# Optimization experiments

Measured on AMD Instinct MI355X. Metric: run time of the kernel, lower is better.

The kernel has to match this reference:

```python
import jax, jax.numpy as jnp
import numpy as np

L = 12      # n_layers
C = 768     # n_embd = dim = dim_att
H = 12      # heads
N = 64      # head_size_a
FF = 2688   # dim_ffn = int(768*3.5//32*32)
P = 2       # patch_size
INCH = 4
IMG = 32
NCLS = 1000
FREQ = 256
HC = C // 2  # conv stem channels (dim//2)
B = 32
D_MIX = 32
D_DEC = 64
LNX_EPS = 1e-5 * 8.0 ** 2  # GroupNorm eps with head_size_divisor=8


def _ln(x, w=None, b=None, eps=1e-5):
    m = x.mean(-1, keepdims=True)
    v = x.var(-1, keepdims=True)
    xh = (x - m) * jax.lax.rsqrt(v + eps)
    if w is not None:
        xh = xh * w + b
    return xh


def _shift(x):  # RWKV token shift: prepend zero row, drop last
    return jnp.pad(x, ((0, 0), (1, 0), (0, 0)))[:, :-1]


def _gn_img(x, w, b, groups=32, eps=1e-5):
    Bb, Ch, Hh, Ww = x.shape
    xg = x.reshape(Bb, groups, Ch // groups, Hh, Ww)
    m = xg.mean((2, 3, 4), keepdims=True)
    v = xg.var((2, 3, 4), keepdims=True)
    xg = (xg - m) * jax.lax.rsqrt(v + eps)
    return xg.reshape(Bb, Ch, Hh, Ww) * w[None, :, None, None] + b[None, :, None, None]


def _conv5(x, w, b):
    y = jax.lax.conv_general_dilated(x, w, (1, 1), ((2, 2), (2, 2)),
                                     dimension_numbers=('NCHW', 'OIHW', 'NCHW'))
    return y + b[None, :, None, None]


def _wkv(r, k, v, w, u):
    # r,k,v,w: (B,T,H,N); u: (H,N). S[b,h,i,j]: key i -> value j.
    def step(S, inp):
        rt, kt, vt, wt = inp  # each (B,H,N)
        kv = kt[..., :, None] * vt[..., None, :]           # (B,H,N,N)
        y = jnp.einsum('bhi,bhij->bhj', rt, S + u[None, :, :, None] * kv)
        S = wt[..., :, None] * S + kv
        return S, y
    S0 = jnp.zeros((r.shape[0], H, N, N), r.dtype)
    seq = tuple(jnp.moveaxis(a, 1, 0) for a in (r, k, v, w))
    _, ys = jax.lax.scan(step, S0, seq)
    return jnp.moveaxis(ys, 0, 1)  # (B,T,H,N)


def _timemix(x, p):
    Bb, Tt, _ = x.shape
    xx = _shift(x) - x
    xxx = x + xx * p['maa'][0]
    mix = jnp.tanh(xxx @ p['tm_w1']).reshape(Bb, Tt, 5, D_MIX)
    m = jnp.einsum('btfd,fdc->fbtc', mix, p['tm_w2'])  # (5,B,T,C): mw,mk,mv,mr,mg
    xw = x + xx * (p['maa'][1] + m[0])
    xk = x + xx * (p['maa'][2] + m[1])
    xv = x + xx * (p['maa'][3] + m[2])
    xr = x + xx * (p['maa'][4] + m[3])
    xg = x + xx * (p['maa'][5] + m[4])
    r = (xr @ p['r_w'].T).reshape(Bb, Tt, H, N)
    k = (xk @ p['k_w'].T).reshape(Bb, Tt, H, N)
    v = (xv @ p['v_w'].T).reshape(Bb, Tt, H, N)
    g = jax.nn.silu(xg @ p['g_w'].T)
    ww = p['td'] + jnp.tanh(xw @ p['td_w1']) @ p['td_w2']
    w = jnp.exp(-jnp.exp(ww)).reshape(Bb, Tt, H, N)
    y = _wkv(r, k, v, w, p['faaaa'])  # (B,T,H,N)
    mn = y.mean(-1, keepdims=True)
    vr = y.var(-1, keepdims=True)
    y = ((y - mn) * jax.lax.rsqrt(vr + LNX_EPS)).reshape(Bb, Tt, C) * p['lnx_w'] + p['lnx_b']
    return (y * g) @ p['o_w'].T


def _chanmix(x, p):
    xx = _shift(x) - x
    xk = x + xx * p['fmaa'][0]
    xr = x + xx * p['fmaa'][1]
    k = jnp.square(jax.nn.relu(xk @ p['fk_w'].T))
    return jax.nn.sigmoid(xr @ p['fr_w'].T) * (k @ p['fv_w'].T)


def _forward(x, t, y, c1_w, c1_b, gn1_w, gn1_b, c2_w, c2_b, gn2_w, gn2_b,
             xe_w, xe_b, te_w1, te_b1, te_w2, te_b2, y_tab, ln0_w, ln0_b,
             ln1_w, ln1_b, ln2_w, ln2_b, att_maa, tm_w1, tm_w2, td, td_w1,
             td_w2, faaaa, r_w, k_w, v_w, o_w, g_w, lnx_w, lnx_b, ffn_maa,
             fk_w, fr_w, fv_w, ada_w, ada_b, fl_ada_w, fl_ada_b, fl_w, fl_b):
    Bb = x.shape[0]
    h = jax.nn.silu(_conv5(x, c1_w, c1_b))
    h = _gn_img(h, gn1_w, gn1_b)
    h = jax.nn.silu(_conv5(h, c2_w, c2_b))
    h = _gn_img(h, gn2_w, gn2_b)
    # patchify: (B,HC,IMG,IMG) -> (B,T,P*P*HC)
    G = IMG // P
    h = h.reshape(Bb, HC, G, P, G, P).transpose(0, 2, 4, 1, 3, 5).reshape(Bb, G * G, HC * P * P)
    xs = h @ xe_w.T + xe_b
    # timestep embedding
    half = FREQ // 2
    freqs = jnp.exp(-jnp.log(10000.0) * jnp.arange(half, dtype=jnp.float32) / half)
    ang = t[:, None] * freqs[None]
    temb = jnp.concatenate([jnp.cos(ang), jnp.sin(ang)], -1)
    temb = jax.nn.silu(temb @ te_w1.T + te_b1) @ te_w2.T + te_b2
    c = temb + y_tab[y]  # adaln_input (B,C)
    for l in range(L):
        ada = jax.nn.silu(c) @ ada_w[l].T + ada_b[l]
        sm, scm, gm, sp, scp, gp = jnp.split(ada, 6, axis=1)
        if l == 0:
            xs = _ln(xs, ln0_w, ln0_b)
        p = dict(maa=att_maa[l], tm_w1=tm_w1[l], tm_w2=tm_w2[l], td=td[l],
                 td_w1=td_w1[l], td_w2=td_w2[l], faaaa=faaaa[l], r_w=r_w[l],
                 k_w=k_w[l], v_w=v_w[l], o_w=o_w[l], g_w=g_w[l], lnx_w=lnx_w[l],
                 lnx_b=lnx_b[l], fmaa=ffn_maa[l], fk_w=fk_w[l], fr_w=fr_w[l],
                 fv_w=fv_w[l])
        hmod = _ln(xs, ln1_w[l], ln1_b[l]) * (1 + scm[:, None, :]) + sm[:, None, :]
        xs = xs + gm[:, None, :] * _timemix(hmod, p)
        hmod = _ln(xs, ln2_w[l], ln2_b[l]) * (1 + scp[:, None, :]) + sp[:, None, :]
        xs = xs + gp[:, None, :] * _chanmix(hmod, p)
    ada = jax.nn.silu(c) @ fl_ada_w.T + fl_ada_b
    sh, sc = jnp.split(ada, 2, axis=1)
    out = (_ln(xs, eps=1e-6) * (1 + sc[:, None, :]) + sh[:, None, :]) @ fl_w.T + fl_b
    G = IMG // P
    out = out.reshape(Bb, G, G, P, P, INCH)
    out = jnp.einsum('nhwpqc->nchpwq', out).reshape(Bb, INCH, IMG, IMG)
    return out


def setup_inputs() -> dict:
    key = jax.random.key(0)
    ks = iter(jax.random.split(key, 64))
    def rn(shape, s=0.02):
        return (jax.random.normal(next(ks), shape) * s).astype(jnp.float32)
    inp = {}
    inp['x'] = jax.random.normal(next(ks), (B, INCH, IMG, IMG), jnp.float32)
    inp['t'] = jax.random.uniform(next(ks), (B,), jnp.float32) * 1000.0
    inp['y'] = jax.random.randint(next(ks), (B,), 0, NCLS)
    inp['c1_w'] = rn((HC, INCH, 5, 5), 0.05); inp['c1_b'] = jnp.zeros(HC)
    inp['gn1_w'] = jnp.ones(HC); inp['gn1_b'] = jnp.zeros(HC)
    inp['c2_w'] = rn((HC, HC, 5, 5), 0.02); inp['c2_b'] = jnp.zeros(HC)
    inp['gn2_w'] = jnp.ones(HC); inp['gn2_b'] = jnp.zeros(HC)
    inp['xe_w'] = rn((C, P * P * HC)); inp['xe_b'] = jnp.zeros(C)
    inp['te_w1'] = rn((C, FREQ)); inp['te_b1'] = jnp.zeros(C)
    inp['te_w2'] = rn((C, C)); inp['te_b2'] = jnp.zeros(C)
    inp['y_tab'] = rn((NCLS + 1, C))
    inp['ln0_w'] = jnp.ones(C); inp['ln0_b'] = jnp.zeros(C)
    inp['ln1_w'] = jnp.ones((L, C)); inp['ln1_b'] = jnp.zeros((L, C))
    inp['ln2_w'] = jnp.ones((L, C)); inp['ln2_b'] = jnp.zeros((L, C))
    inp['att_maa'] = jax.random.uniform(next(ks), (L, 6, C), jnp.float32)
    inp['tm_w1'] = rn((L, C, 5 * D_MIX), 0.01)
    inp['tm_w2'] = rn((L, 5, D_MIX, C), 0.01)
    inp['td'] = rn((L, C), 0.5) - 3.0
    inp['td_w1'] = rn((L, C, D_DEC), 0.01)
    inp['td_w2'] = rn((L, D_DEC, C), 0.01)
    inp['faaaa'] = rn((L, H, N), 0.1)
    for nm in ('r_w', 'k_w', 'v_w', 'o_w', 'g_w'):
        inp[nm] = rn((L, C, C))
    inp['lnx_w'] = jnp.ones((L, C)); inp['lnx_b'] = jnp.zeros((L, C))
    inp['ffn_maa'] = jax.random.uniform(next(ks), (L, 2, C), jnp.float32)
    inp['fk_w'] = rn((L, FF, C)); inp['fr_w'] = rn((L, C, C)); inp['fv_w'] = rn((L, C, FF))
    inp['ada_w'] = rn((L, 6 * C, C)); inp['ada_b'] = jnp.zeros((L, 6 * C))
    inp['fl_ada_w'] = rn((2 * C, C)); inp['fl_ada_b'] = jnp.zeros(2 * C)
    inp['fl_w'] = rn((P * P * INCH, C)); inp['fl_b'] = jnp.zeros(P * P * INCH)
    return inp


def reference(x, t, y, c1_w, c1_b, gn1_w, gn1_b, c2_w, c2_b, gn2_w, gn2_b,
              xe_w, xe_b, te_w1, te_b1, te_w2, te_b2, y_tab, ln0_w, ln0_b,
              ln1_w, ln1_b, ln2_w, ln2_b, att_maa, tm_w1, tm_w2, td, td_w1,
              td_w2, faaaa, r_w, k_w, v_w, o_w, g_w, lnx_w, lnx_b, ffn_maa,
              fk_w, fr_w, fv_w, ada_w, ada_b, fl_ada_w, fl_ada_b, fl_w, fl_b):
    return _forward(x, t, y, c1_w, c1_b, gn1_w, gn1_b, c2_w, c2_b, gn2_w, gn2_b,
                    xe_w, xe_b, te_w1, te_b1, te_w2, te_b2, y_tab, ln0_w, ln0_b,
                    ln1_w, ln1_b, ln2_w, ln2_b, att_maa, tm_w1, tm_w2, td, td_w1,
                    td_w2, faaaa, r_w, k_w, v_w, o_w, g_w, lnx_w, lnx_b, ffn_maa,
                    fk_w, fr_w, fv_w, ada_w, ada_b, fl_ada_w, fl_ada_b, fl_w, fl_b)
```

## Files before the change

### kernel.cpp

```cpp
#include <hip/hip_runtime.h>
#include <math.h>


typedef short  s16x8 __attribute__((ext_vector_type(8)));
typedef float  f32x4 __attribute__((ext_vector_type(4)));
typedef __attribute__((address_space(1))) const void as1_cv;
typedef __attribute__((address_space(3))) void as3_v;

#define GLDS16(gp, lp) __builtin_amdgcn_global_load_lds( \
    (as1_cv*)(unsigned long long)(const void*)(gp), \
    (as3_v*)(unsigned int)(unsigned long long)(void*)(lp), 16, 0, 0)

static __device__ __forceinline__ float sigf(float x){ return 1.f/(1.f+expf(-x)); }
static __device__ __forceinline__ unsigned short f2b(float x){
  unsigned int u = __builtin_bit_cast(unsigned int, x);
  unsigned int r = (u + 0x7FFFu + ((u >> 16) & 1u)) >> 16;
  return (unsigned short)r;
}
static __device__ __forceinline__ float b2f(unsigned short h){
  unsigned int u = ((unsigned int)h)<<16; return __builtin_bit_cast(float,u);
}

static const size_t O_XS    = 0ull;
static const size_t O_HMOD  = 6291456ull;
static const size_t O_ADA   = 12582912ull;
static const size_t O_FLA   = 14352384ull;
static const size_t O_T2    = 14401536ull;
static const size_t O_SC    = 14426112ull;
static const size_t O_TI    = 14450688ull;
static const size_t O_T1    = 14458880ull;
static const size_t O_ST1   = 14483456ull;
static const size_t O_ST2   = 14485504ull;
static const size_t O_XEW16 = 14487552ull;
static const size_t O_WL16  = 15077376ull;
static const size_t O_BIG   = 19083264ull;
static const size_t L_XW    = 0ull;
static const size_t L_XX    = 6291456ull;
static const size_t L_XXX   = 12582912ull;
static const size_t L_KB    = 18874368ull;
static const size_t L_VB    = 25165824ull;
static const size_t L_GB    = 31457280ull;
static const size_t L_WD    = 37748736ull;
static const size_t L_MIXB  = 50331648ull;
static const size_t L_WT    = 51642368ull;
static const size_t L_XK16  = 52166656ull;
static const size_t L_XV16  = 55312384ull;
static const size_t L_XR16  = 58458112ull;
static const size_t L_XG16  = 61603840ull;
static const size_t L_GNH16 = 64749568ull;
static const size_t L_KBIG16= 67895296ull;
static const size_t S_IMG1  = 0ull;
static const size_t S_IMG2  = 12582912ull;
static const size_t S_PAD16 = 25165824ull;
static const size_t S_WTAP16= 33128448ull;
static const size_t S_PM16  = 34971648ull;

enum { EPI_NONE=0, EPI_SILU=1 };

template<int EPI, bool TB>
__global__ __launch_bounds__(256) void gemm_k(
    const float* __restrict__ A, const float* __restrict__ B,
    float* __restrict__ C, const float* __restrict__ bias,
    int M, int N, int K)
{
  __shared__ __align__(16) float As[16][68];
  __shared__ __align__(16) float Bs[16][68];
  const int tid = threadIdx.x;
  const int tx = tid & 15, ty = tid >> 4;
  const int row0 = blockIdx.y * 64, col0 = blockIdx.x * 64;
  const int lr = tid >> 2;
  const int lk = (tid & 3) << 2;
  float acc[4][4] = {};
  for (int k0 = 0; k0 < K; k0 += 16) {
    {
      int gr = row0 + lr;
      float4 v = make_float4(0.f,0.f,0.f,0.f);
      if (gr < M) v = *reinterpret_cast<const float4*>(A + (size_t)gr*K + (k0 + lk));
      As[lk+0][lr]=v.x; As[lk+1][lr]=v.y; As[lk+2][lr]=v.z; As[lk+3][lr]=v.w;
    }
    if (TB) {
      int gr = col0 + lr;
      float4 v = make_float4(0.f,0.f,0.f,0.f);
      if (gr < N) v = *reinterpret_cast<const float4*>(B + (size_t)gr*K + (k0 + lk));
      Bs[lk+0][lr]=v.x; Bs[lk+1][lr]=v.y; Bs[lk+2][lr]=v.z; Bs[lk+3][lr]=v.w;
    } else {
      int kr = tid >> 4;
      int gc = col0 + ((tid & 15) << 2);
      float4 v = make_float4(0.f,0.f,0.f,0.f);
      if (gc < N) v = *reinterpret_cast<const float4*>(B + (size_t)(k0+kr)*N + gc);
      Bs[kr][((tid&15)<<2)+0]=v.x; Bs[kr][((tid&15)<<2)+1]=v.y;
      Bs[kr][((tid&15)<<2)+2]=v.z; Bs[kr][((tid&15)<<2)+3]=v.w;
    }
    __syncthreads();
    #pragma unroll
    for (int kk=0;kk<16;kk++){
      const float4 a4 = *reinterpret_cast<const float4*>(&As[kk][ty<<2]);
      const float4 b4 = *reinterpret_cast<const float4*>(&Bs[kk][tx<<2]);
      const float av[4]={a4.x,a4.y,a4.z,a4.w};
      const float bv[4]={b4.x,b4.y,b4.z,b4.w};
      #pragma unroll
      for (int i=0;i<4;i++)
        #pragma unroll
        for (int j=0;j<4;j++)
          acc[i][j]=fmaf(av[i],bv[j],acc[i][j]);
    }
    __syncthreads();
  }
  #pragma unroll
  for (int i=0;i<4;i++){
    const int r = row0 + (ty<<2) + i;
    if (r >= M) break;
    #pragma unroll
    for (int j=0;j<4;j++){
      const int c = col0 + (tx<<2) + j;
      if (c >= N) break;
      float v = acc[i][j];
      if (bias) v += bias[c];
      const size_t idx = (size_t)r*N + c;
      if (EPI==EPI_NONE)        C[idx]=v;
      else if (EPI==EPI_SILU)   C[idx]=v*sigf(v);
    }
  }
}

#define GEMM(EPI,TB,A,B,C,bias,M,N,K) \
  gemm_k<EPI,TB><<<dim3(((N)+63)/64,((M)+63)/64),dim3(256),0,stream>>>((A),(B),(C),(bias),(M),(N),(K))

enum { BEPI_F32=0, BEPI_BIAS_F32, BEPI_SILU_F32, BEPI_SIG_F32, BEPI_RELU2_BF16,
       BEPI_RES_GM, BEPI_RES_GP, BEPI_TANH_BF16, BEPI_WDEC_F32 };

template<int EPI>
__global__ __launch_bounds__(256) void bgemm_k(
    const unsigned short* __restrict__ A, const unsigned short* __restrict__ B,
    void* __restrict__ Cv, const float* __restrict__ bias,
    const float* __restrict__ p1, const float* __restrict__ p2, int pstride,
    int M, int N, int K)
{
  __shared__ __align__(16) unsigned short As[128][64];
  __shared__ __align__(16) unsigned short Bs[128][64];
  const int tid = threadIdx.x;
  const int w = tid >> 6, lane = tid & 63;
  const int row0 = blockIdx.y * 128, col0 = blockIdx.x * 128;
  const int wr = w >> 1, wc = w & 1;
  const int l15 = lane & 15, l4 = lane >> 4;
  const int kkc = ((lane & 7) ^ (lane >> 3)) * 8;
  f32x4 acc[4][4] = {};
  for (int k0 = 0; k0 < K; k0 += 64) {
    #pragma unroll
    for (int i = 0; i < 4; i++) {
      const int rb = i*32 + w*8;
      const int r  = rb + (lane >> 3);
      GLDS16(A + (size_t)(row0 + r)*K + k0 + kkc, &As[rb][0]);
      GLDS16(B + (size_t)(col0 + r)*K + k0 + kkc, &Bs[rb][0]);
    }
    __syncthreads();
    #pragma unroll
    for (int ks = 0; ks < 2; ks++) {
      s16x8 af[4], bf[4];
      #pragma unroll
      for (int m = 0; m < 4; m++) {
        const int r = wr*64 + m*16 + l15;
        const int sl = (ks*4 + l4) ^ (r & 7);
        af[m] = *reinterpret_cast<const s16x8*>(&As[r][sl*8]);
      }
      #pragma unroll
      for (int n = 0; n < 4; n++) {
        const int r = wc*64 + n*16 + l15;
        const int sl = (ks*4 + l4) ^ (r & 7);
        bf[n] = *reinterpret_cast<const s16x8*>(&Bs[r][sl*8]);
      }
      #pragma unroll
      for (int m = 0; m < 4; m++)
        #pragma unroll
        for (int n = 0; n < 4; n++)
          acc[m][n] = __builtin_amdgcn_mfma_f32_16x16x32_bf16(af[m], bf[n], acc[m][n], 0, 0, 0);
    }
    __syncthreads();
  }
  float* Cf = (float*)Cv; unsigned short* Ch = (unsigned short*)Cv;
  #pragma unroll
  for (int m = 0; m < 4; m++) {
    const int rbase = row0 + wr*64 + m*16 + (l4<<2);
    #pragma unroll
    for (int n = 0; n < 4; n++) {
      const int c = col0 + wc*64 + n*16 + l15;
      if (c >= N) continue;
      #pragma unroll
      for (int q = 0; q < 4; q++) {
        const int r = rbase + q;
        const int bb = r >> 8;
        float v = acc[m][n][q];
        const size_t idx = (size_t)r*N + c;
        if (EPI==BEPI_F32)            Cf[idx] = v;
        else if (EPI==BEPI_BIAS_F32)  Cf[idx] = v + bias[c];
        else if (EPI==BEPI_SILU_F32)  Cf[idx] = v*sigf(v);
        else if (EPI==BEPI_SIG_F32)   Cf[idx] = sigf(v);
        else if (EPI==BEPI_RELU2_BF16){ float t=fmaxf(v,0.f); Ch[idx] = f2b(t*t); }
        else if (EPI==BEPI_RES_GM)    Cf[idx] += p1[(size_t)bb*pstride + c]*v;
        else if (EPI==BEPI_RES_GP)    Cf[idx] += p1[(size_t)bb*pstride + c]*(p2[idx]*v);
        else if (EPI==BEPI_TANH_BF16) Ch[idx] = f2b(tanhf(v));
        else if (EPI==BEPI_WDEC_F32)  Cf[idx] = expf(-expf(v + p1[c]));
      }
    }
  }
}

#define BGEMM(EPI,A16,B16,Cp,bias,p1,p2,ps,M,N,K) \
  bgemm_k<EPI><<<dim3(((N)+127)/128,(M)/128),dim3(256),0,stream>>>( \
    (const unsigned short*)(A16),(const unsigned short*)(B16),(void*)(Cp),(bias),(p1),(p2),(ps),(M),(N),(K))

struct BGrp { const unsigned short* A; const unsigned short* B; void* C;
              int epi; int N; int gx; };
struct BGrp4 { BGrp g[4]; };

__global__ __launch_bounds__(256) void bgemm_grp_k(BGrp4 G, int M, int K)
{
  const BGrp gr = G.g[blockIdx.z];
  if ((int)blockIdx.x >= gr.gx) return;
  __shared__ __align__(16) unsigned short As[128][64];
  __shared__ __align__(16) unsigned short Bs[128][64];
  const int tid = threadIdx.x;
  const int w = tid >> 6, lane = tid & 63;
  const int row0 = blockIdx.y * 128, col0 = blockIdx.x * 128;
  const int wr = w >> 1, wc = w & 1;
  const int l15 = lane & 15, l4 = lane >> 4;
  const int kkc = ((lane & 7) ^ (lane >> 3)) * 8;
  const int N = gr.N;
  f32x4 acc[4][4] = {};
  for (int k0 = 0; k0 < K; k0 += 64) {
    #pragma unroll
    for (int i = 0; i < 4; i++) {
      const int rb = i*32 + w*8;
      const int r  = rb + (lane >> 3);
      GLDS16(gr.A + (size_t)(row0 + r)*K + k0 + kkc, &As[rb][0]);
      GLDS16(gr.B + (size_t)(col0 + r)*K + k0 + kkc, &Bs[rb][0]);
    }
    __syncthreads();
    #pragma unroll
    for (int ks = 0; ks < 2; ks++) {
      s16x8 af[4], bf[4];
      #pragma unroll
      for (int m = 0; m < 4; m++) {
        const int r = wr*64 + m*16 + l15;
        const int sl = (ks*4 + l4) ^ (r & 7);
        af[m] = *reinterpret_cast<const s16x8*>(&As[r][sl*8]);
      }
      #pragma unroll
      for (int n = 0; n < 4; n++) {
        const int r = wc*64 + n*16 + l15;
        const int sl = (ks*4 + l4) ^ (r & 7);
        bf[n] = *reinterpret_cast<const s16x8*>(&Bs[r][sl*8]);
      }
      #pragma unroll
      for (int m = 0; m < 4; m++)
        #pragma unroll
        for (int n = 0; n < 4; n++)
          acc[m][n] = __builtin_amdgcn_mfma_f32_16x16x32_bf16(af[m], bf[n], acc[m][n], 0, 0, 0);
    }
    __syncthreads();
  }
  float* Cf = (float*)gr.C; unsigned short* Ch = (unsigned short*)gr.C;
  #pragma unroll
  for (int m = 0; m < 4; m++) {
    const int rbase = row0 + wr*64 + m*16 + (l4<<2);
    #pragma unroll
    for (int n = 0; n < 4; n++) {
      const int c = col0 + wc*64 + n*16 + l15;
      #pragma unroll
      for (int q = 0; q < 4; q++) {
        const int r = rbase + q;
        float v = acc[m][n][q];
        const size_t idx = (size_t)r*N + c;
        switch (gr.epi) {
          case 0: Cf[idx] = v; break;
          case 1: Cf[idx] = v*sigf(v); break;
          case 2: Cf[idx] = sigf(v); break;
          case 3: { float t=fmaxf(v,0.f); Ch[idx] = f2b(t*t); } break;
          case 4: Ch[idx] = f2b(v); break;
          default: Ch[idx] = f2b(v*sigf(v)); break;
        }
      }
    }
  }
}

__global__ __launch_bounds__(256) void conv1_k(
    const float* __restrict__ x, const float* __restrict__ w,
    const float* __restrict__ bias, float* __restrict__ out)
{
  const int blk = blockIdx.x; const int bb = blk / 384; const int oc = blk % 384;
  __shared__ __align__(16) float sIn[4*1296];
  __shared__ __align__(16) float sW[100];
  const int tid = threadIdx.x;
  for (int idx=tid; idx<4*1296; idx+=256){
    int ic = idx/1296; int rem = idx - ic*1296;
    int yy = rem/36, xx = rem - yy*36;
    int gy = yy-2, gx = xx-2;
    float v = 0.f;
    if ((unsigned)gy < 32u && (unsigned)gx < 32u)
      v = x[(((size_t)bb*4+ic)*32+gy)*32+gx];
    sIn[idx]=v;
  }
  if (tid < 100) sW[tid] = w[(size_t)oc*100 + tid];
  __syncthreads();
  const float bv = bias[oc];
  #pragma unroll
  for (int i=0;i<4;i++){
    int p = tid + 256*i; int py=p>>5, px=p&31;
    int pb = py*36+px;
    float acc = bv;
    #pragma unroll
    for (int ic=0;ic<4;ic++)
      #pragma unroll
      for (int ky=0;ky<5;ky++)
        #pragma unroll
        for (int kx=0;kx<5;kx++)
          acc = fmaf(sIn[ic*1296 + pb + ky*36+kx], sW[ic*25+ky*5+kx], acc);
    out[((size_t)(bb*384+oc))*1024 + p] = acc*sigf(acc);
  }
}

__global__ __launch_bounds__(256) void gn_stats_nchw_k(
    const float* __restrict__ h, float* __restrict__ stats)
{
  const int blk = blockIdx.x;
  const size_t base = (size_t)blk*12288;
  const int tid = threadIdx.x;
  float s=0.f, s2=0.f;
  for (int idx=tid; idx<12288; idx+=256){ float v=h[base+idx]; s+=v; s2=fmaf(v,v,s2); }
  #pragma unroll
  for (int mask=32; mask>=1; mask>>=1){ s += __shfl_xor(s,mask); s2 += __shfl_xor(s2,mask); }
  __shared__ float ps[8];
// ... 5 lines not shown
    float var  = s2*(1.f/12288.f) - mean*mean;
    stats[blk*2] = mean; stats[blk*2+1] = rsqrtf(var + 1e-5f);
  }
}

__global__ void zero16_k(unsigned short* __restrict__ p)
{
  size_t i = ((size_t)blockIdx.x*256 + threadIdx.x)*8;
  *reinterpret_cast<uint4*>(p + i) = make_uint4(0u,0u,0u,0u);
}

__global__ __launch_bounds__(256) void pad_apply_k(
    const float* __restrict__ img1, const float* __restrict__ stats,
    const float* __restrict__ w, const float* __restrict__ bgn,
    unsigned short* __restrict__ pad)
{
  __shared__ float t[8][33];
  const int b = blockIdx.x >> 5, y = blockIdx.x & 31;
  const int tid = threadIdx.x;
  for (int ic0 = 0; ic0 < 384; ic0 += 8) {
    const int icr = tid >> 5, xr = tid & 31;
    t[icr][xr] = img1[(((size_t)b*384 + ic0+icr)*32 + y)*32 + xr];
    __syncthreads();
    const int xw_ = tid >> 3, icw = tid & 7;
    const int ch = ic0 + icw;
    const int g = ch / 12;
    const float mean = stats[(b*32+g)*2], rstd = stats[(b*32+g)*2+1];
    float v = (t[icw][xw_] - mean)*rstd*w[ch] + bgn[ch];
    pad[(((size_t)b*36 + y+2)*36 + (xw_+2))*384 + ch] = f2b(v);
    __syncthreads();
  }
}

__global__ __launch_bounds__(256) void wrepack_k(
    const float* __restrict__ w, unsigned short* __restrict__ wtap)
{
  __shared__ float t[9600];
  const int oc = blockIdx.x; const int tid = threadIdx.x;
  for (int i=tid;i<9600;i+=256) t[i] = w[(size_t)oc*9600 + i];
  __syncthreads();
  for (int i=tid;i<9600;i+=256){
    int tap=i/384, ic=i-tap*384;
    wtap[((size_t)tap*384 + oc)*384 + ic] = f2b(t[ic*25+tap]);
  }
}

__global__ __launch_bounds__(256) void conv2m_k(
    const unsigned short* __restrict__ inp,
    const unsigned short* __restrict__ wtap,
    const float* __restrict__ bias, unsigned short* __restrict__ out)
{
  __shared__ __align__(16) unsigned short As[128][64];
  __shared__ __align__(16) unsigned short Bs[128][64];
  const int blk = blockIdx.x;
  const int b = blk / 24, rem = blk % 24, pt = rem / 3, ot = rem % 3;
  const int y0 = pt * 4, oc0 = ot * 128;
  const int tid = threadIdx.x, w = tid>>6, lane = tid&63;
  const int wr = w>>1, wc = w&1;
  const int l15 = lane & 15, l4 = lane >> 4;
  const int kkc = ((lane&7) ^ (lane>>3)) * 8;
  f32x4 acc[4][4] = {};
  for (int ic0 = 0; ic0 < 384; ic0 += 64) {
    for (int dy = 0; dy < 5; dy++) {
      for (int dx = 0; dx < 5; dx++) {
        const int tap = dy*5 + dx;
        #pragma unroll
        for (int i = 0; i < 4; i++) {
          const int rb = i*32 + w*8;
          const int r = rb + (lane>>3);
          const int py = r >> 5, px = r & 31;
          GLDS16(inp + (((size_t)(b*36 + y0+py+dy))*36 + (px+dx))*384 + ic0 + kkc, &As[rb][0]);
          GLDS16(wtap + ((size_t)tap*384 + oc0 + r)*384 + ic0 + kkc, &Bs[rb][0]);
        }
        __syncthreads();
        #pragma unroll
        for (int ks = 0; ks < 2; ks++) {
          s16x8 af[4], bf[4];
          #pragma unroll
          for (int m = 0; m < 4; m++) {
            const int r = wr*64 + m*16 + l15;
            const int sl = (ks*4 + l4) ^ (r & 7);
            af[m] = *reinterpret_cast<const s16x8*>(&As[r][sl*8]);
          }
          #pragma unroll
          for (int n = 0; n < 4; n++) {
            const int r = wc*64 + n*16 + l15;
            const int sl = (ks*4 + l4) ^ (r & 7);
            bf[n] = *reinterpret_cast<const s16x8*>(&Bs[r][sl*8]);
          }
          #pragma unroll
          for (int m = 0; m < 4; m++)
            #pragma unroll
            for (int n = 0; n < 4; n++)
              acc[m][n] = __builtin_amdgcn_mfma_f32_16x16x32_bf16(af[m], bf[n], acc[m][n], 0, 0, 0);
        }
        __syncthreads();
      }
    }
  }
  #pragma unroll
  for (int m = 0; m < 4; m++) {
    #pragma unroll
    for (int n = 0; n < 4; n++) {
      const int oc = oc0 + wc*64 + n*16 + l15;
      const float bv = bias[oc];
      #pragma unroll
      for (int q = 0; q < 4; q++) {
        const int p = wr*64 + m*16 + (l4<<2) + q;
// ... 148 lines not shown
__global__ __launch_bounds__(256) void ln_shift_cm_k(
    const float* __restrict__ xs, const float* __restrict__ w, const float* __restrict__ b,
    const float* __restrict__ mod, const float* __restrict__ fmaa,
    unsigned short* __restrict__ xk16, unsigned short* __restrict__ xr16)
{
  const int m = blockIdx.x, tid = threadIdx.x;
  const size_t base = (size_t)m*768;
  const int t = m & 255, bb = m >> 8;
  float c0=xs[base+tid], c1=xs[base+tid+256], c2=xs[base+tid+512];
  float p0=0.f,p1=0.f,p2=0.f;
  if (t) { p0=xs[base-768+tid]; p1=xs[base-512+tid]; p2=xs[base-256+tid]; }
  float sc_=c0+c1+c2, sc2=fmaf(c0,c0,fmaf(c1,c1,c2*c2));
  float sp_=p0+p1+p2, sp2=fmaf(p0,p0,fmaf(p1,p1,p2*p2));
  #pragma unroll
  for (int mask=32; mask>=1; mask>>=1){
    sc_+=__shfl_xor(sc_,mask); sc2+=__shfl_xor(sc2,mask);
    sp_+=__shfl_xor(sp_,mask); sp2+=__shfl_xor(sp2,mask);
  }
  __shared__ float ps[16];
  if ((tid&63)==0){ int wv=tid>>6; ps[wv]=sc_; ps[4+wv]=sc2; ps[8+wv]=sp_; ps[12+wv]=sp2; }
  __syncthreads();
  sc_=ps[0]+ps[1]+ps[2]+ps[3]; sc2=ps[4]+ps[5]+ps[6]+ps[7];
  sp_=ps[8]+ps[9]+ps[10]+ps[11]; sp2=ps[12]+ps[13]+ps[14]+ps[15];
  const float mc = sc_*(1.f/768.f), rc = rsqrtf(sc2*(1.f/768.f)-mc*mc + 1e-5f);
  const float mp = sp_*(1.f/768.f), rp = rsqrtf(sp2*(1.f/768.f)-mp*mp + 1e-5f);
  #pragma unroll
  for (int k=0;k<3;k++){
    const int c = tid + k*256;
    const float scv = mod[(size_t)bb*55296 + 3072 + c];
    const float shv = mod[(size_t)bb*55296 + 2304 + c];
    float cv = (k==0)?c0:((k==1)?c1:c2);
    float h = fmaf((cv-mc)*rc, w[c], b[c]);
    h = fmaf(h, 1.f+scv, shv);
    float pv = 0.f;
    if (t) {
      float pk = (k==0)?p0:((k==1)?p1:p2);
      pv = fmaf((pk-mp)*rp, w[c], b[c]);
      pv = fmaf(pv, 1.f+scv, shv);
    }
    const float d = pv - h;
    xk16[base+c] = f2b(fmaf(d, fmaa[c], h));
    xr16[base+c] = f2b(fmaf(d, fmaa[768+c], h));
  }
}

__global__ __launch_bounds__(256) void five_mix_k(
    const unsigned short* __restrict__ mix16, const float* __restrict__ w2,
    const float* __restrict__ hmod, const float* __restrict__ xx,
    const float* __restrict__ maa15,
    unsigned short* __restrict__ xw, unsigned short* __restrict__ xk,
    unsigned short* __restrict__ xv, unsigned short* __restrict__ xr,
    unsigned short* __restrict__ xg)
{
  __shared__ __align__(16) float smix[16][160];
  const int m0 = blockIdx.x * 16;
  const int tid = threadIdx.x;
  for (int idx=tid; idx<16*160; idx+=256){
    int r = idx/160, d = idx - r*160;
    smix[r][d] = b2f(mix16[(size_t)(m0+r)*160 + d]);
  }
  __syncthreads();
  #pragma unroll 1
  for (int cc=0; cc<3; cc++){
    const int c = tid + cc*256;
    float hv[16], xv_[16];
    #pragma unroll
    for (int r=0;r<16;r++){ size_t id=(size_t)(m0+r)*768+c; hv[r]=hmod[id]; xv_[r]=xx[id]; }
    #pragma unroll 1
    for (int f=0; f<5; f++){
      float acc[16];
      const float base = maa15[f*768 + c];
      #pragma unroll
      for (int r=0;r<16;r++) acc[r]=base;
      #pragma unroll 1
      for (int d4=0; d4<8; d4++){
        float wv[4];
        #pragma unroll
        for (int q=0;q<4;q++) wv[q] = w2[(size_t)(f*32+d4*4+q)*768 + c];
        #pragma unroll
        for (int r=0;r<16;r++){
          const float4 mv = *reinterpret_cast<const float4*>(&smix[r][f*32+d4*4]);
          acc[r] = fmaf(mv.x,wv[0],fmaf(mv.y,wv[1],fmaf(mv.z,wv[2],fmaf(mv.w,wv[3],acc[r]))));
        }
      }
      #pragma unroll
      for (int r=0;r<16;r++){
        float val = fmaf(xv_[r], acc[r], hv[r]);
        size_t id = (size_t)(m0+r)*768+c;
        if (f==0) xw[id]=f2b(val);
        else if (f==1) xk[id]=f2b(val);
        else if (f==2) xv[id]=f2b(val);
        else if (f==3) xr[id]=f2b(val);
        else           xg[id]=f2b(val);
      }
    }
  }
}

__global__ __launch_bounds__(256) void wkv_k(
    const unsigned short* __restrict__ rg, const unsigned short* __restrict__ kg,
    const unsigned short* __restrict__ vg, const float* __restrict__ wg,
    const unsigned short* __restrict__ gg, const float* __restrict__ u,
    const float* __restrict__ lnxw, const float* __restrict__ lnxb,
    unsigned short* __restrict__ out16)
{
  const int bh = blockIdx.x; const int b = bh/12, h = bh%12;
  const int tid = threadIdx.x;
  const int w = tid >> 6, lane = tid & 63;
  const int l4 = lane >> 4, l15 = lane & 15;
  __shared__ __align__(16) unsigned short r16s[32][64], k16s[32][64], v16s[32][64], g16s[32][64];
  __shared__ __align__(16) float wds[32][64];
  __shared__ __align__(16) float Wl[33][64];
  __shared__ __align__(16) unsigned short rr16[32][64], kk16[32][64];
  __shared__ __align__(16) unsigned short kk2T[64][32], vT[64][32];
  __shared__ __align__(16) unsigned short S16T[64][64];
  __shared__ __align__(16) unsigned short A16[32][32];
  __shared__ float diag[32], ypsum[32][4], ypsq[32][4];

  reinterpret_cast<uint4*>(&S16T[0][0])[tid] = make_uint4(0,0,0,0);
  reinterpret_cast<uint4*>(&S16T[0][0])[256+tid] = make_uint4(0,0,0,0);

  const float u_lane = u[h*64 + lane];
  const int jj = w*16 + l15;
  const float lw = lnxw[h*64 + jj], lb = lnxb[h*64 + jj];
  const size_t gb = (size_t)(b*256)*768 + h*64;

  const int st_t = tid >> 3, st_i = (tid & 7) * 8;
  uint4 pr, pk, pv, pg; float4 pw0, pw1;

#define WKV_LOADC(c_) { \
    const size_t tb = gb + (size_t)((c_)*32 + st_t)*768 + st_i; \
    pr = *reinterpret_cast<const uint4*>(rg + tb); \
    pk = *reinterpret_cast<const uint4*>(kg + tb); \
    pv = *reinterpret_cast<const uint4*>(vg + tb); \
    pg = *reinterpret_cast<const uint4*>(gg + tb); \
    pw0 = *reinterpret_cast<const float4*>(wg + tb); \
    pw1 = *reinterpret_cast<const float4*>(wg + tb + 4); }
#define WKV_STAGE() { \
    *reinterpret_cast<uint4*>(&r16s[st_t][st_i]) = pr; \
// ... 126 lines not shown
    }
    #pragma unroll
    for (int m=0;m<2;m++)
      #pragma unroll
      for (int q=0;q<4;q++){
        float s1 = Y[m][q], s2 = s1*s1;
        #pragma unroll
        for (int mask=8; mask>=1; mask>>=1){ s1 += __shfl_xor(s1,mask); s2 += __shfl_xor(s2,mask); }
        if (l15==0){ const int t = m*16 + l4*4 + q; ypsum[t][w]=s1; ypsq[t][w]=s2; }
      }
    __syncthreads();
    #pragma unroll
    for (int m=0;m<2;m++)
      #pragma unroll
      for (int q=0;q<4;q++){
        const int t = m*16 + l4*4 + q;
        float s1 = ypsum[t][0]+ypsum[t][1]+ypsum[t][2]+ypsum[t][3];
        float s2 = ypsq[t][0]+ypsq[t][1]+ypsq[t][2]+ypsq[t][3];
        float mean = s1*(1.f/64.f);
        float var  = s2*(1.f/64.f) - mean*mean;
        float xh = (Y[m][q]-mean)*rsqrtf(var + 6.4e-4f);
        float o = fmaf(xh, lw, lb) * b2f(g16s[t][jj]);
        out16[gb + (size_t)(c*32+t)*768 + jj] = f2b(o);
      }
    if (c < 7) {
      __syncthreads();
      WKV_STAGE();
      __syncthreads();
    }
  }
#undef WKV_LOADC
#undef WKV_STAGE
}

__global__ void unpatch_k(const float* __restrict__ po, float* __restrict__ out)
{
  int idx = blockIdx.x*256 + threadIdx.x;
  int xq=idx&31; int yy=(idx>>5)&31; int ch=(idx>>10)&3; int bb=idx>>12;
  int gh=yy>>1, p=yy&1, gw=xq>>1, q=xq&1;
  out[idx] = po[((size_t)(bb*256+gh*16+gw))*16 + p*8+q*4+ch];
}

__global__ void f2b_k(const float* __restrict__ s, unsigned short* __restrict__ d)
{
  size_t i = ((size_t)blockIdx.x*256 + threadIdx.x)*8;
  float4 a = *reinterpret_cast<const float4*>(s+i);
  float4 b = *reinterpret_cast<const float4*>(s+i+4);
  s16x8 o;
  o[0]=(short)f2b(a.x); o[1]=(short)f2b(a.y); o[2]=(short)f2b(a.z); o[3]=(short)f2b(a.w);
  o[4]=(short)f2b(b.x); o[5]=(short)f2b(b.y); o[6]=(short)f2b(b.z); o[7]=(short)f2b(b.w);
  *reinterpret_cast<s16x8*>(d + i) = o;
}

__global__ void f2b_layer_k(
    const float* __restrict__ r_, const float* __restrict__ k_, const float* __restrict__ v_,
    const float* __restrict__ o_, const float* __restrict__ g_, const float* __restrict__ fr_,
    const float* __restrict__ fk_, const float* __restrict__ fv_,
    unsigned short* __restrict__ dst)
{
  size_t i = ((size_t)blockIdx.x*256 + threadIdx.x)*8;
  const float* s; size_t off;
  if (i < 3538944) {
    unsigned seg = (unsigned)(i / 589824u); off = i - (size_t)seg*589824u;
    s = seg==0?r_:seg==1?k_:seg==2?v_:seg==3?o_:seg==4?g_:fr_;
  } else if (i < 5603328) { s = fk_; off = i - 3538944; }
  else                    { s = fv_; off = i - 5603328; }
  float4 a = *reinterpret_cast<const float4*>(s+off);
  float4 b = *reinterpret_cast<const float4*>(s+off+4);
  s16x8 o;
  o[0]=(short)f2b(a.x); o[1]=(short)f2b(a.y); o[2]=(short)f2b(a.z); o[3]=(short)f2b(a.w);
  o[4]=(short)f2b(b.x); o[5]=(short)f2b(b.y); o[6]=(short)f2b(b.z); o[7]=(short)f2b(b.w);
  *reinterpret_cast<s16x8*>(dst + i) = o;
}

__global__ void wmix_repack_k(const float* __restrict__ tm1, const float* __restrict__ td1,
                              const float* __restrict__ td2, unsigned short* __restrict__ dst)
{
  int idx = blockIdx.x*256 + threadIdx.x;
  if (idx < 196608) {
    int n = idx/768, k = idx - n*768;
    dst[idx] = (n<160) ? f2b(tm1[(size_t)k*160 + n]) : (unsigned short)0;
  } else if (idx < 294912) {
    int i = idx-196608; int n = i/768, k = i - n*768;
    dst[idx] = (n<64) ? f2b(td1[(size_t)k*64 + n]) : (unsigned short)0;
  } else {
    int i = idx-294912; int n = i/64, k = i - n*64;
    dst[idx] = f2b(td2[(size_t)k*768 + n]);
  }
}

extern "C" void kernel_launch(void* const* d_in, const int* in_sizes, int n_in,
                              void* d_out, int out_size, void* d_ws, size_t ws_size,
                              hipStream_t stream)
{
  const float* x_in  = (const float*)d_in[0];
  const float* t_in  = (const float*)d_in[1];
  const int*   y_in  = (const int*)  d_in[2];
  const float* c1w   = (const float*)d_in[3];
  const float* c1b   = (const float*)d_in[4];
  const float* gn1w  = (const float*)d_in[5];
  const float* gn1b  = (const float*)d_in[6];
  const float* c2w   = (const float*)d_in[7];
  const float* c2b   = (const float*)d_in[8];
  const float* gn2w  = (const float*)d_in[9];
  const float* gn2b  = (const float*)d_in[10];
  const float* xew   = (const float*)d_in[11];
  const float* xeb   = (const float*)d_in[12];
  const float* tew1  = (const float*)d_in[13];
  const float* teb1  = (const float*)d_in[14];
  const float* tew2  = (const float*)d_in[15];
  const float* teb2  = (const float*)d_in[16];
  const float* ytab  = (const float*)d_in[17];
  const float* ln0w  = (const float*)d_in[18];
  const float* ln0b  = (const float*)d_in[19];
  const float* ln1w  = (const float*)d_in[20];
  const float* ln1b  = (const float*)d_in[21];
  const float* ln2w  = (const float*)d_in[22];
  const float* ln2b  = (const float*)d_in[23];
  const float* amaa  = (const float*)d_in[24];
  const float* tmw1  = (const float*)d_in[25];
  const float* tmw2  = (const float*)d_in[26];
  const float* tdv   = (const float*)d_in[27];
  const float* tdw1  = (const float*)d_in[28];
  const float* tdw2  = (const float*)d_in[29];
  const float* faa   = (const float*)d_in[30];
  const float* rw    = (const float*)d_in[31];
  const float* kw    = (const float*)d_in[32];
  const float* vw    = (const float*)d_in[33];
  const float* ow    = (const float*)d_in[34];
  const float* gw    = (const float*)d_in[35];
  const float* lnxw  = (const float*)d_in[36];
  const float* lnxb  = (const float*)d_in[37];
  const float* fmaa  = (const float*)d_in[38];
  const float* fkw   = (const float*)d_in[39];
  const float* frw   = (const float*)d_in[40];
  const float* fvw   = (const float*)d_in[41];
  const float* adaw  = (const float*)d_in[42];
  const float* adab  = (const float*)d_in[43];
  const float* flaw  = (const float*)d_in[44];
  const float* flab  = (const float*)d_in[45];
  const float* flw   = (const float*)d_in[46];
  const float* flb   = (const float*)d_in[47];

  float* Wf = (float*)d_ws;
  float* xs   = Wf+O_XS;   float* hmod = Wf+O_HMOD;
  float* ada  = Wf+O_ADA;  float* fla  = Wf+O_FLA;
  float* t2   = Wf+O_T2;   float* sc   = Wf+O_SC;
  float* ti   = Wf+O_TI;   float* t1   = Wf+O_T1;
  float* st1  = Wf+O_ST1;  float* st2  = Wf+O_ST2;
  unsigned short* xew16 = (unsigned short*)(Wf+O_XEW16);
  unsigned short* wl16  = (unsigned short*)(Wf+O_WL16);
  float* big = Wf+O_BIG;
  float* xxb  = big+L_XX;
  float* wd   = big+L_WD;
  float* gbf  = big+L_GB;
  unsigned short* rb16  = (unsigned short*)(big+L_XXX);
  unsigned short* kb16  = (unsigned short*)(big+L_KB);
  unsigned short* vb16  = (unsigned short*)(big+L_VB);
  unsigned short* gb16  = (unsigned short*)(big+L_GB);
  unsigned short* xw16  = (unsigned short*)(big+L_XW);
  unsigned short* xxx16 = (unsigned short*)(big+L_XXX);
  unsigned short* mixb16= (unsigned short*)(big+L_MIXB);
  unsigned short* wt16  = (unsigned short*)(big+L_WT);
  unsigned short* xk16 = (unsigned short*)(big+L_XK16);
  unsigned short* xv16 = (unsigned short*)(big+L_XV16);
  unsigned short* xr16 = (unsigned short*)(big+L_XR16);
  unsigned short* xg16 = (unsigned short*)(big+L_XG16);
  unsigned short* gnh16 = (unsigned short*)(big+L_GNH16);
  unsigned short* kbig16 = (unsigned short*)(big+L_KBIG16);
  float* img1 = big+S_IMG1;
  unsigned short* img2_16 = (unsigned short*)(big+S_IMG2);
  unsigned short* pad16  = (unsigned short*)(big+S_PAD16);
  unsigned short* wtap16 = (unsigned short*)(big+S_WTAP16);
  unsigned short* pm16   = (unsigned short*)(big+S_PM16);
  float* pout = big+L_MIXB;
  unsigned short* dr  = wl16;
  unsigned short* dk  = wl16 + 589824;
  unsigned short* dv  = wl16 + 1179648;
  unsigned short* do_ = wl16 + 1769472;
  unsigned short* dg  = wl16 + 2359296;
  unsigned short* dfr = wl16 + 2949120;
  unsigned short* dfk = wl16 + 3538944;
  unsigned short* dfv = wl16 + 5603328;
  unsigned short* dtm1t = wl16 + 7667712;
  unsigned short* dtd1t = wl16 + 7864320;
  unsigned short* dtd2t = wl16 + 7962624;

  conv1_k<<<dim3(32*384),dim3(256),0,stream>>>(x_in, c1w, c1b, img1);
  gn_stats_nchw_k<<<dim3(1024),dim3(256),0,stream>>>(img1, st1);
  zero16_k<<<dim3(7776),dim3(256),0,stream>>>(pad16);
  pad_apply_k<<<dim3(1024),dim3(256),0,stream>>>(img1, st1, gn1w, gn1b, pad16);
  wrepack_k<<<dim3(384),dim3(256),0,stream>>>(c2w, wtap16);
  conv2m_k<<<dim3(768),dim3(256),0,stream>>>(pad16, wtap16, c2b, img2_16);
  gn_stats_nhwc_k<<<dim3(1024),dim3(256),0,stream>>>(img2_16, st2);
  patchify_gn_k<<<dim3(49152),dim3(256),0,stream>>>(img2_16, st2, gn2w, gn2b, pm16);
  f2b_k<<<dim3(576),dim3(256),0,stream>>>(xew, xew16);
  BGEMM(BEPI_BIAS_F32, pm16, xew16, xs, xeb, nullptr,nullptr,0, 8192,768,1536);

  temb_in_k<<<dim3(32),dim3(128),0,stream>>>(t_in, ti);
  GEMM(EPI_SILU,true, ti, tew1, t1, teb1, 32,768,256);
  GEMM(EPI_NONE,true, t1, tew2, t2, teb2, 32,768,768);
  siluc_k<<<dim3(32),dim3(256),0,stream>>>(t2, ytab, y_in, sc);
  GEMM(EPI_NONE,true, sc, adaw, ada, adab, 32,55296,768);
  GEMM(EPI_NONE,true, sc, flaw, fla, flab, 32,1536,768);

  ln_mod_k<<<dim3(8192),dim3(256),0,stream>>>(xs, xs, ln0w, ln0b, nullptr, 0,0,0, 1e-5f);

  for (int l=0; l<12; l++){
    const float* adal = ada + (size_t)l*4608;
    f2b_layer_k<<<dim3(3744),dim3(256),0,stream>>>(
        rw+(size_t)l*589824, kw+(size_t)l*589824, vw+(size_t)l*589824,
        ow+(size_t)l*589824, gw+(size_t)l*589824, frw+(size_t)l*589824,
        fkw+(size_t)l*2064384, fvw+(size_t)l*2064384, wl16);
    wmix_repack_k<<<dim3(1344),dim3(256),0,stream>>>(
        tmw1+(size_t)l*122880, tdw1+(size_t)l*49152, tdw2+(size_t)l*49152, dtm1t);
    ln_shift_tm_k<<<dim3(8192),dim3(256),0,stream>>>(
        xs, ln1w+(size_t)l*768, ln1b+(size_t)l*768, adal, amaa+(size_t)l*4608,
        hmod, xxb, xxx16);
    BGEMM(BEPI_TANH_BF16, xxx16, dtm1t, mixb16, nullptr,nullptr,nullptr,0, 8192,160,768);
    five_mix_k<<<dim3(512),dim3(256),0,stream>>>(mixb16, tmw2+(size_t)l*122880, hmod, xxb,
                                                 amaa+(size_t)l*4608+768, xw16,xk16,xv16,xr16,xg16);
    BGEMM(BEPI_TANH_BF16, xw16, dtd1t, wt16, nullptr,nullptr,nullptr,0, 8192,64,768);
    BGEMM(BEPI_WDEC_F32, wt16, dtd2t, wd, nullptr, tdv+(size_t)l*768, nullptr,0, 8192,768,64);
    {
      BGrp4 G;
      G.g[0].A=xr16; G.g[0].B=dr; G.g[0].C=rb16; G.g[0].epi=4; G.g[0].N=768; G.g[0].gx=6;
      G.g[1].A=xk16; G.g[1].B=dk; G.g[1].C=kb16; G.g[1].epi=4; G.g[1].N=768; G.g[1].gx=6;
      G.g[2].A=xv16; G.g[2].B=dv; G.g[2].C=vb16; G.g[2].epi=4; G.g[2].N=768; G.g[2].gx=6;
      G.g[3].A=xg16; G.g[3].B=dg; G.g[3].C=gb16; G.g[3].epi=5; G.g[3].N=768; G.g[3].gx=6;
      bgemm_grp_k<<<dim3(6,64,4),dim3(256),0,stream>>>(G, 8192, 768);
    }
    wkv_k<<<dim3(384),dim3(256),0,stream>>>(rb16, kb16, vb16, wd, gb16, faa+(size_t)l*768,
                                            lnxw+(size_t)l*768, lnxb+(size_t)l*768, gnh16);
    BGEMM(BEPI_RES_GM, gnh16, do_, xs, nullptr, adal+1536, nullptr, 55296, 8192,768,768);
    ln_shift_cm_k<<<dim3(8192),dim3(256),0,stream>>>(
        xs, ln2w+(size_t)l*768, ln2b+(size_t)l*768, adal, fmaa+(size_t)l*1536, xk16, xr16);
    {
      BGrp4 G;
      G.g[0].A=xk16; G.g[0].B=dfk; G.g[0].C=kbig16; G.g[0].epi=3; G.g[0].N=2688; G.g[0].gx=21;
      G.g[1].A=xr16; G.g[1].B=dfr; G.g[1].C=gbf;    G.g[1].epi=2; G.g[1].N=768;  G.g[1].gx=6;
      G.g[2]=G.g[1]; G.g[3]=G.g[1];
      bgemm_grp_k<<<dim3(21,64,2),dim3(256),0,stream>>>(G, 8192, 768);
    }
    BGEMM(BEPI_RES_GP, kbig16, dfv, xs, nullptr, adal+3840, gbf, 55296, 8192,768,2688);
  }

  ln_mod_k<<<dim3(8192),dim3(256),0,stream>>>(xs, hmod, nullptr, nullptr, fla, 1536, 0, 768, 1e-6f);
  GEMM(EPI_NONE,true, hmod, flw, pout, flb, 8192,16,768);
  unpatch_k<<<dim3(512),dim3(256),0,stream>>>(pout, (float*)d_out);
}
```

Baseline: 8.418 ms.

## Fuse decay GEMM into grouped GEMM, merge weight conversion kernels, bf16 gate

Several unrelated changes land together. The time-decay first-stage GEMM becomes a fifth group in the grouped r/k/v/g GEMM, and the second-stage decay GEMM runs with K padded to 128 instead of 64. The per-layer weight bf16 conversion and the mix-weight repack are merged into one launch. The channel-mix sigmoid gate is stored as bf16 instead of fp32, halving its write and read traffic. five_mix uses 8-row blocks for more parallelism, and the conv block index is remapped for better locality. The bf16 gate adds rounding error, and the padded K does extra MFMA work on zeros.

```diff
diff --git a/kernel.cpp b/kernel.cpp
--- a/kernel.cpp
+++ b/kernel.cpp
@@ -33,7 +33,7 @@
 static const size_t O_ST2   = 14485504ull;
 static const size_t O_XEW16 = 14487552ull;
 static const size_t O_WL16  = 15077376ull;
-static const size_t O_BIG   = 19083264ull;
+static const size_t O_BIG   = 19107840ull;
 static const size_t L_XW    = 0ull;
 static const size_t L_XX    = 6291456ull;
 static const size_t L_XXX   = 12582912ull;
@@ -127,13 +127,13 @@
   gemm_k<EPI,TB><<<dim3(((N)+63)/64,((M)+63)/64),dim3(256),0,stream>>>((A),(B),(C),(bias),(M),(N),(K))
 
 enum { BEPI_F32=0, BEPI_BIAS_F32, BEPI_SILU_F32, BEPI_SIG_F32, BEPI_RELU2_BF16,
-       BEPI_RES_GM, BEPI_RES_GP, BEPI_TANH_BF16, BEPI_WDEC_F32 };
+       BEPI_RES_GM, BEPI_RES_GP16, BEPI_TANH_BF16, BEPI_WDEC_F32 };
 
 template<int EPI>
 __global__ __launch_bounds__(256) void bgemm_k(
     const unsigned short* __restrict__ A, const unsigned short* __restrict__ B,
     void* __restrict__ Cv, const float* __restrict__ bias,
-    const float* __restrict__ p1, const float* __restrict__ p2, int pstride,
+    const float* __restrict__ p1, const void* __restrict__ p2, int pstride,
     int M, int N, int K)
 {
   __shared__ __align__(16) unsigned short As[128][64];
@@ -178,6 +178,7 @@
     __syncthreads();
   }
   float* Cf = (float*)Cv; unsigned short* Ch = (unsigned short*)Cv;
+  const unsigned short* p2h = (const unsigned short*)p2;
   #pragma unroll
   for (int m = 0; m < 4; m++) {
     const int rbase = row0 + wr*64 + m*16 + (l4<<2);
@@ -197,7 +198,7 @@
         else if (EPI==BEPI_SIG_F32)   Cf[idx] = sigf(v);
         else if (EPI==BEPI_RELU2_BF16){ float t=fmaxf(v,0.f); Ch[idx] = f2b(t*t); }
         else if (EPI==BEPI_RES_GM)    Cf[idx] += p1[(size_t)bb*pstride + c]*v;
-        else if (EPI==BEPI_RES_GP)    Cf[idx] += p1[(size_t)bb*pstride + c]*(p2[idx]*v);
+        else if (EPI==BEPI_RES_GP16)  Cf[idx] += p1[(size_t)bb*pstride + c]*(b2f(p2h[idx])*v);
         else if (EPI==BEPI_TANH_BF16) Ch[idx] = f2b(tanhf(v));
         else if (EPI==BEPI_WDEC_F32)  Cf[idx] = expf(-expf(v + p1[c]));
       }
@@ -211,9 +212,9 @@
 
 struct BGrp { const unsigned short* A; const unsigned short* B; void* C;
               int epi; int N; int gx; };
-struct BGrp4 { BGrp g[4]; };
-
-__global__ __launch_bounds__(256) void bgemm_grp_k(BGrp4 G, int M, int K)
+struct BGrp5 { BGrp g[5]; };
+
+__global__ __launch_bounds__(256) void bgemm_grp_k(BGrp5 G, int M, int K)
 {
   const BGrp gr = G.g[blockIdx.z];
   if ((int)blockIdx.x >= gr.gx) return;
@@ -274,10 +275,11 @@
         switch (gr.epi) {
           case 0: Cf[idx] = v; break;
           case 1: Cf[idx] = v*sigf(v); break;
-          case 2: Cf[idx] = sigf(v); break;
           case 3: { float t=fmaxf(v,0.f); Ch[idx] = f2b(t*t); } break;
           case 4: Ch[idx] = f2b(v); break;
-          default: Ch[idx] = f2b(v*sigf(v)); break;
+          case 5: Ch[idx] = f2b(v*sigf(v)); break;
+          case 6: Ch[idx] = f2b(tanhf(v)); break;
+          default: Ch[idx] = f2b(sigf(v)); break;
         }
       }
     }
@@ -389,8 +391,9 @@
 {
   __shared__ __align__(16) unsigned short As[128][64];
   __shared__ __align__(16) unsigned short Bs[128][64];
-  const int blk = blockIdx.x;
-  const int b = blk / 24, rem = blk % 24, pt = rem / 3, ot = rem % 3;
+  const int s = (blockIdx.x % 8) * 96 + blockIdx.x / 8;
+  const int ot = s / 256; const int rem = s % 256;
+  const int b = rem >> 3, pt = rem & 7;
   const int y0 = pt * 4, oc0 = ot * 128;
   const int tid = threadIdx.x, w = tid>>6, lane = tid&63;
   const int wr = w>>1, wc = w&1;
@@ -645,10 +648,10 @@
     unsigned short* __restrict__ xv, unsigned short* __restrict__ xr,
     unsigned short* __restrict__ xg)
 {
-  __shared__ __align__(16) float smix[16][160];
-  const int m0 = blockIdx.x * 16;
+  __shared__ __align__(16) float smix[8][160];
+  const int m0 = blockIdx.x * 8;
   const int tid = threadIdx.x;
-  for (int idx=tid; idx<16*160; idx+=256){
+  for (int idx=tid; idx<8*160; idx+=256){
     int r = idx/160, d = idx - r*160;
     smix[r][d] = b2f(mix16[(size_t)(m0+r)*160 + d]);
   }
@@ -656,28 +659,28 @@
   #pragma unroll 1
   for (int cc=0; cc<3; cc++){
     const int c = tid + cc*256;
-    float hv[16], xv_[16];
-    #pragma unroll
-    for (int r=0;r<16;r++){ size_t id=(size_t)(m0+r)*768+c; hv[r]=hmod[id]; xv_[r]=xx[id]; }
+    float hv[8], xv_[8];
+    #pragma unroll
+    for (int r=0;r<8;r++){ size_t id=(size_t)(m0+r)*768+c; hv[r]=hmod[id]; xv_[r]=xx[id]; }
     #pragma unroll 1
     for (int f=0; f<5; f++){
-      float acc[16];
+      float acc[8];
       const float base = maa15[f*768 + c];
       #pragma unroll
-      for (int r=0;r<16;r++) acc[r]=base;
+      for (int r=0;r<8;r++) acc[r]=base;
       #pragma unroll 1
       for (int d4=0; d4<8; d4++){
         float wv[4];
         #pragma unroll
         for (int q=0;q<4;q++) wv[q] = w2[(size_t)(f*32+d4*4+q)*768 + c];
         #pragma unroll
-        for (int r=0;r<16;r++){
+        for (int r=0;r<8;r++){
           const float4 mv = *reinterpret_cast<const float4*>(&smix[r][f*32+d4*4]);
           acc[r] = fmaf(mv.x,wv[0],fmaf(mv.y,wv[1],fmaf(mv.z,wv[2],fmaf(mv.w,wv[3],acc[r]))));
         }
       }
       #pragma unroll
-      for (int r=0;r<16;r++){
+      for (int r=0;r<8;r++){
         float val = fmaf(xv_[r], acc[r], hv[r]);
         size_t id = (size_t)(m0+r)*768+c;
         if (f==0) xw[id]=f2b(val);
@@ -910,40 +913,40 @@
   *reinterpret_cast<s16x8*>(d + i) = o;
 }
 
-__global__ void f2b_layer_k(
+__global__ void f2bw_layer_k(
     const float* __restrict__ r_, const float* __restrict__ k_, const float* __restrict__ v_,
     const float* __restrict__ o_, const float* __restrict__ g_, const float* __restrict__ fr_,
     const float* __restrict__ fk_, const float* __restrict__ fv_,
+    const float* __restrict__ tm1, const float* __restrict__ td1, const float* __restrict__ td2,
     unsigned short* __restrict__ dst)
 {
-  size_t i = ((size_t)blockIdx.x*256 + threadIdx.x)*8;
-  const float* s; size_t off;
-  if (i < 3538944) {
-    unsigned seg = (unsigned)(i / 589824u); off = i - (size_t)seg*589824u;
-    s = seg==0?r_:seg==1?k_:seg==2?v_:seg==3?o_:seg==4?g_:fr_;
-  } else if (i < 5603328) { s = fk_; off = i - 3538944; }
-  else                    { s = fv_; off = i - 5603328; }
-  float4 a = *reinterpret_cast<const float4*>(s+off);
-  float4 b = *reinterpret_cast<const float4*>(s+off+4);
-  s16x8 o;
-  o[0]=(short)f2b(a.x); o[1]=(short)f2b(a.y); o[2]=(short)f2b(a.z); o[3]=(short)f2b(a.w);
-  o[4]=(short)f2b(b.x); o[5]=(short)f2b(b.y); o[6]=(short)f2b(b.z); o[7]=(short)f2b(b.w);
-  *reinterpret_cast<s16x8*>(dst + i) = o;
-}
-
-__global__ void wmix_repack_k(const float* __restrict__ tm1, const float* __restrict__ td1,
-                              const float* __restrict__ td2, unsigned short* __restrict__ dst)
-{
-  int idx = blockIdx.x*256 + threadIdx.x;
-  if (idx < 196608) {
-    int n = idx/768, k = idx - n*768;
-    dst[idx] = (n<160) ? f2b(tm1[(size_t)k*160 + n]) : (unsigned short)0;
-  } else if (idx < 294912) {
-    int i = idx-196608; int n = i/768, k = i - n*768;
-    dst[idx] = (n<64) ? f2b(td1[(size_t)k*64 + n]) : (unsigned short)0;
+  if (blockIdx.x < 3744) {
+    size_t i = ((size_t)blockIdx.x*256 + threadIdx.x)*8;
+    const float* s; size_t off;
+    if (i < 3538944) {
+      unsigned seg = (unsigned)(i / 589824u); off = i - (size_t)seg*589824u;
+      s = seg==0?r_:seg==1?k_:seg==2?v_:seg==3?o_:seg==4?g_:fr_;
+    } else if (i < 5603328) { s = fk_; off = i - 3538944; }
+    else                    { s = fv_; off = i - 5603328; }
+    float4 a = *reinterpret_cast<const float4*>(s+off);
+    float4 b = *reinterpret_cast<const float4*>(s+off+4);
+    s16x8 o;
+    o[0]=(short)f2b(a.x); o[1]=(short)f2b(a.y); o[2]=(short)f2b(a.z); o[3]=(short)f2b(a.w);
+    o[4]=(short)f2b(b.x); o[5]=(short)f2b(b.y); o[6]=(short)f2b(b.z); o[7]=(short)f2b(b.w);
+    *reinterpret_cast<s16x8*>(dst + i) = o;
   } else {
-    int i = idx-294912; int n = i/64, k = i - n*64;
-    dst[idx] = f2b(td2[(size_t)k*768 + n]);
+    int idx = (blockIdx.x-3744)*256 + threadIdx.x;
+    unsigned short* rp = dst + 7667712;
+    if (idx < 196608) {
+      int n = idx/768, k = idx - n*768;
+      rp[idx] = (n<160) ? f2b(tm1[(size_t)k*160 + n]) : (unsigned short)0;
+    } else if (idx < 294912) {
+      int i = idx-196608; int n = i/768, k = i - n*768;
+      rp[idx] = (n<64) ? f2b(td1[(size_t)k*64 + n]) : (unsigned short)0;
+    } else {
+      int i = idx-294912; int n = i/128, kk = i & 127;
+      rp[idx] = (kk<64) ? f2b(td2[(size_t)kk*768 + n]) : (unsigned short)0;
+    }
   }
 }
 
@@ -1011,7 +1014,6 @@
   float* big = Wf+O_BIG;
   float* xxb  = big+L_XX;
   float* wd   = big+L_WD;
-  float* gbf  = big+L_GB;
   unsigned short* rb16  = (unsigned short*)(big+L_XXX);
   unsigned short* kb16  = (unsigned short*)(big+L_KB);
   unsigned short* vb16  = (unsigned short*)(big+L_VB);
@@ -1066,41 +1068,40 @@
 
   for (int l=0; l<12; l++){
     const float* adal = ada + (size_t)l*4608;
-    f2b_layer_k<<<dim3(3744),dim3(256),0,stream>>>(
+    f2bw_layer_k<<<dim3(5280),dim3(256),0,stream>>>(
         rw+(size_t)l*589824, kw+(size_t)l*589824, vw+(size_t)l*589824,
         ow+(size_t)l*589824, gw+(size_t)l*589824, frw+(size_t)l*589824,
-        fkw+(size_t)l*2064384, fvw+(size_t)l*2064384, wl16);
-    wmix_repack_k<<<dim3(1344),dim3(256),0,stream>>>(
-        tmw1+(size_t)l*122880, tdw1+(size_t)l*49152, tdw2+(size_t)l*49152, dtm1t);
+        fkw+(size_t)l*2064384, fvw+(size_t)l*2064384,
+        tmw1+(size_t)l*122880, tdw1+(size_t)l*49152, tdw2+(size_t)l*49152, wl16);
     ln_shift_tm_k<<<dim3(8192),dim3(256),0,stream>>>(
         xs, ln1w+(size_t)l*768, ln1b+(size_t)l*768, adal, amaa+(size_t)l*4608,
         hmod, xxb, xxx16);
     BGEMM(BEPI_TANH_BF16, xxx16, dtm1t, mixb16, nullptr,nullptr,nullptr,0, 8192,160,768);
-    five_mix_k<<<dim3(512),dim3(256),0,stream>>>(mixb16, tmw2+(size_t)l*122880, hmod, xxb,
-                                                 amaa+(size_t)l*4608+768, xw16,xk16,xv16,xr16,xg16);
-    BGEMM(BEPI_TANH_BF16, xw16, dtd1t, wt16, nullptr,nullptr,nullptr,0, 8192,64,768);
-    BGEMM(BEPI_WDEC_F32, wt16, dtd2t, wd, nullptr, tdv+(size_t)l*768, nullptr,0, 8192,768,64);
+    five_mix_k<<<dim3(1024),dim3(256),0,stream>>>(mixb16, tmw2+(size_t)l*122880, hmod, xxb,
+                                                  amaa+(size_t)l*4608+768, xw16,xk16,xv16,xr16,xg16);
     {
-      BGrp4 G;
-      G.g[0].A=xr16; G.g[0].B=dr; G.g[0].C=rb16; G.g[0].epi=4; G.g[0].N=768; G.g[0].gx=6;
-      G.g[1].A=xk16; G.g[1].B=dk; G.g[1].C=kb16; G.g[1].epi=4; G.g[1].N=768; G.g[1].gx=6;
-      G.g[2].A=xv16; G.g[2].B=dv; G.g[2].C=vb16; G.g[2].epi=4; G.g[2].N=768; G.g[2].gx=6;
-      G.g[3].A=xg16; G.g[3].B=dg; G.g[3].C=gb16; G.g[3].epi=5; G.g[3].N=768; G.g[3].gx=6;
-      bgemm_grp_k<<<dim3(6,64,4),dim3(256),0,stream>>>(G, 8192, 768);
-    }
+      BGrp5 G;
+      G.g[0].A=xr16; G.g[0].B=dr;    G.g[0].C=rb16; G.g[0].epi=4; G.g[0].N=768; G.g[0].gx=6;
+      G.g[1].A=xk16; G.g[1].B=dk;    G.g[1].C=kb16; G.g[1].epi=4; G.g[1].N=768; G.g[1].gx=6;
+      G.g[2].A=xv16; G.g[2].B=dv;    G.g[2].C=vb16; G.g[2].epi=4; G.g[2].N=768; G.g[2].gx=6;
+      G.g[3].A=xg16; G.g[3].B=dg;    G.g[3].C=gb16; G.g[3].epi=5; G.g[3].N=768; G.g[3].gx=6;
+      G.g[4].A=xw16; G.g[4].B=dtd1t; G.g[4].C=wt16; G.g[4].epi=6; G.g[4].N=128; G.g[4].gx=1;
+      bgemm_grp_k<<<dim3(6,64,5),dim3(256),0,stream>>>(G, 8192, 768);
+    }
+    BGEMM(BEPI_WDEC_F32, wt16, dtd2t, wd, nullptr, tdv+(size_t)l*768, nullptr,0, 8192,768,128);
     wkv_k<<<dim3(384),dim3(256),0,stream>>>(rb16, kb16, vb16, wd, gb16, faa+(size_t)l*768,
                                             lnxw+(size_t)l*768, lnxb+(size_t)l*768, gnh16);
     BGEMM(BEPI_RES_GM, gnh16, do_, xs, nullptr, adal+1536, nullptr, 55296, 8192,768,768);
     ln_shift_cm_k<<<dim3(8192),dim3(256),0,stream>>>(
         xs, ln2w+(size_t)l*768, ln2b+(size_t)l*768, adal, fmaa+(size_t)l*1536, xk16, xr16);
     {
-      BGrp4 G;
+      BGrp5 G;
       G.g[0].A=xk16; G.g[0].B=dfk; G.g[0].C=kbig16; G.g[0].epi=3; G.g[0].N=2688; G.g[0].gx=21;
-      G.g[1].A=xr16; G.g[1].B=dfr; G.g[1].C=gbf;    G.g[1].epi=2; G.g[1].N=768;  G.g[1].gx=6;
-      G.g[2]=G.g[1]; G.g[3]=G.g[1];
+      G.g[1].A=xr16; G.g[1].B=dfr; G.g[1].C=gb16;   G.g[1].epi=7; G.g[1].N=768;  G.g[1].gx=6;
+      G.g[2]=G.g[1]; G.g[3]=G.g[1]; G.g[4]=G.g[1];
       bgemm_grp_k<<<dim3(21,64,2),dim3(256),0,stream>>>(G, 8192, 768);
     }
-    BGEMM(BEPI_RES_GP, kbig16, dfv, xs, nullptr, adal+3840, gbf, 55296, 8192,768,2688);
+    BGEMM(BEPI_RES_GP16, kbig16, dfv, xs, nullptr, adal+3840, gb16, 55296, 8192,768,2688);
   }
 
   ln_mod_k<<<dim3(8192),dim3(256),0,stream>>>(xs, hmod, nullptr, nullptr, fla, 1536, 0, 768, 1e-6f);
```

After: 9.043 ms. 7.4% more time.
